# Performance work log

Hardware: AMD Instinct MI355X
Metric: run time of the kernel (lower is better)

## Reference

```python
import jax, jax.numpy as jnp
import numpy as np

N_NODES = 50000
N_EDGES = 800000
ALPHA = 0.2  # LeakyReLU negative slope


def setup_inputs() -> dict:
    key = jax.random.key(0)
    ks = jax.random.split(key, 12)
    F_IN, H, D, NOUT = 256, 8, 64, 64

    def xavier(k, shape):
        fan_in, fan_out = shape[-2], shape[-1]
        limit = np.sqrt(6.0 / (fan_in + fan_out)).astype(np.float32)
        return jax.random.uniform(k, shape, jnp.float32, -limit, limit)

    x = jax.random.normal(ks[0], (N_NODES, F_IN), jnp.float32)
    edge_src = jnp.sort(jax.random.randint(ks[1], (N_EDGES,), 0, N_NODES, jnp.int32))
    edge_dst = jax.random.randint(ks[2], (N_EDGES,), 0, N_NODES, jnp.int32)
    return {
        'x': x,
        'edge_src': edge_src,
        'edge_dst': edge_dst,
        'W1': xavier(ks[3], (H, F_IN, D)),
        'a_src1': xavier(ks[4], (H, D, 1))[..., 0],
        'a_dst1': xavier(ks[5], (H, D, 1))[..., 0],
        'W2': xavier(ks[6], (H, H * D, D)),
        'a_src2': xavier(ks[7], (H, D, 1))[..., 0],
        'a_dst2': xavier(ks[8], (H, D, 1))[..., 0],
        'lin_W': xavier(ks[9], (H * D, NOUT)),
        'lin_b': jnp.zeros((NOUT,), jnp.float32),
    }


def _gat_layer(x, W, a_s, a_d, src, dst, n_nodes):
    # W: [H, F, D]; x: [N, F]
    Wh = jnp.einsum('nf,hfd->nhd', x, W)                  # [N, H, D]
    f1 = jnp.einsum('nhd,hd->nh', Wh, a_s)                # score from row node
    f2 = jnp.einsum('nhd,hd->nh', Wh, a_d)                # score from col node
    e = f1[src] + f2[dst]                                 # [E, H]
    e = jnp.where(e > 0, e, ALPHA * e)                    # LeakyReLU
    # sparse softmax over neighbors of each row (dim=1 in torch.sparse.softmax)
    m = jax.ops.segment_max(e, src, num_segments=n_nodes)
    m = jnp.where(jnp.isfinite(m), m, 0.0)                # guard empty segments
    p = jnp.exp(e - m[src])
    s = jax.ops.segment_sum(p, src, num_segments=n_nodes)
    att = p / jnp.maximum(s[src], 1e-16)                  # [E, H]
    # spmm: per-head to cap the [E, D] message buffer
    H = W.shape[0]
    outs = []
    for h in range(H):
        msg = att[:, h:h + 1] * Wh[dst, h, :]             # [E, D]
        outs.append(jax.ops.segment_sum(msg, src, num_segments=n_nodes))
    hp = jnp.stack(outs, axis=1)                          # [N, H, D]
    hp = jax.nn.elu(hp)
    return hp.reshape(n_nodes, -1)                        # concat heads -> [N, H*D]


def reference(x, edge_src, edge_dst, W1, a_src1, a_dst1, W2, a_src2, a_dst2, lin_W, lin_b):
    n = x.shape[0]
    h = _gat_layer(x, W1, a_src1, a_dst1, edge_src, edge_dst, n)
    h = _gat_layer(h, W2, a_src2, a_dst2, edge_src, edge_dst, n)
    return h @ lin_W + lin_b                              # [N, nout]
```

## Files before the change

### kernel.cpp

```cpp
#include <hip/hip_runtime.h>
#include <hip/hip_bf16.h>
#include <math.h>

#define ALPHA 0.2f
#define N_NODES 50000
#define N_EDGES 800000
#define HEADS 8
#define DH 64
#define HD 512
#define DCAP 128

typedef __attribute__((ext_vector_type(8))) short short8v;
typedef __attribute__((ext_vector_type(4))) float float4v;

__device__ __forceinline__ unsigned short f2bf(float f) {
    unsigned int u = __float_as_uint(f);
    unsigned int r = (u + 0x7fffu + ((u >> 16) & 1u)) >> 16;
    return (unsigned short)r;
}
__device__ __forceinline__ float bf2f(unsigned short h) {
    return __uint_as_float(((unsigned int)h) << 16);
}

__device__ __forceinline__ void gl_lds16(const unsigned short* g, unsigned short* l) {
    __builtin_amdgcn_global_load_lds(
        (const __attribute__((address_space(1))) unsigned int*)(g),
        (__attribute__((address_space(3))) unsigned int*)(l),
        16, 0, 0);
}

__global__ void build_rowptr(const int* __restrict__ src, int E, int n_nodes,
                             int* __restrict__ row_ptr) {
    int n = blockIdx.x * blockDim.x + threadIdx.x;
    if (n > n_nodes) return;
    int lo = 0, hi = E;
    while (lo < hi) {
        int mid = (lo + hi) >> 1;
        if (src[mid] < n) lo = mid + 1; else hi = mid;
    }
    row_ptr[n] = lo;
}

__global__ __launch_bounds__(256) void cast_bf16(
    const float* __restrict__ in, unsigned short* __restrict__ out, int total8) {
    int i = blockIdx.x * 256 + threadIdx.x;
    if (i >= total8) return;
    const float4* p = reinterpret_cast<const float4*>(in + (size_t)i * 8);
    float4 v0 = p[0], v1 = p[1];
    float vv[8] = {v0.x, v0.y, v0.z, v0.w, v1.x, v1.y, v1.z, v1.w};
    short8v o;
    #pragma unroll
    for (int q = 0; q < 8; ++q) o[q] = (short)f2bf(vv[q]);
    *reinterpret_cast<short8v*>(out + (size_t)i * 8) = o;
}

__global__ void transpose_w_bf(const float* __restrict__ in,
                               unsigned short* __restrict__ outB,
                               int F, int total) {
    int idx = blockIdx.x * 256 + threadIdx.x;
    if (idx >= total) return;
    int d = idx & 63;
    int f = (idx >> 6) % F;
    int h = idx / (F << 6);
    outB[(size_t)((h << 6) + d) * F + f] = f2bf(in[idx]);
}

__global__ __launch_bounds__(256) void gemm_bf16(
    const unsigned short* __restrict__ A,
    const unsigned short* __restrict__ B,
    const float* __restrict__ bias,
    float* __restrict__ C, unsigned short* __restrict__ Cbf,
    int M, int K, int N)
{
    __shared__ unsigned short As[128][64];
    __shared__ unsigned short Bs[128][64];

    const int tid = threadIdx.x;
    const int bm = blockIdx.x * 128;
    const int bn = blockIdx.y * 128;
    const int wid = tid >> 6;
    const int lane = tid & 63;

    const int wr = (wid >> 1) * 64;
    const int wc = (wid & 1) * 64;
    const int fr = lane & 15;
    const int fks = (lane >> 4) * 8;

    const int a_r = lane >> 3;
    const int a_c = 8 * ((lane & 7) ^ a_r);

    float4v acc[4][4];
    #pragma unroll
    for (int m = 0; m < 4; ++m)
        #pragma unroll
        for (int n = 0; n < 4; ++n)
            acc[m][n] = (float4v){0.f, 0.f, 0.f, 0.f};

    for (int k0 = 0; k0 < K; k0 += 64) {
        #pragma unroll
        for (int i = 0; i < 4; ++i) {
            int g = wid * 4 + i;
            int row = bm + g * 8 + a_r; if (row >= M) row = M - 1;
            gl_lds16(&A[(size_t)row * K + k0 + a_c], &As[g * 8][0]);
        }
        #pragma unroll
        for (int i = 0; i < 4; ++i) {
            int g = wid * 4 + i;
            int row = bn + g * 8 + a_r; if (row >= N) row = N - 1;
            gl_lds16(&B[(size_t)row * K + k0 + a_c], &Bs[g * 8][0]);
        }
        __syncthreads();

        #pragma unroll
        for (int ks = 0; ks < 2; ++ks) {
            const int fko = ks * 32 + fks;
            short8v aF[4], bF[4];
            #pragma unroll
            for (int m = 0; m < 4; ++m) {
                int rr = wr + m * 16 + fr;
                aF[m] = *reinterpret_cast<const short8v*>(&As[rr][fko ^ ((rr & 7) * 8)]);
            }
            #pragma unroll
            for (int n = 0; n < 4; ++n) {
                int cc = wc + n * 16 + fr;
                bF[n] = *reinterpret_cast<const short8v*>(&Bs[cc][fko ^ ((cc & 7) * 8)]);
            }
            #pragma unroll
            for (int m = 0; m < 4; ++m)
                #pragma unroll
                for (int n = 0; n < 4; ++n)
                    acc[m][n] = __builtin_amdgcn_mfma_f32_16x16x32_bf16(aF[m], bF[n], acc[m][n], 0, 0, 0);
        }
        __syncthreads();
    }

    #pragma unroll
    for (int m = 0; m < 4; ++m) {
        int row0 = bm + wr + m * 16 + (lane >> 4) * 4;
        #pragma unroll
        for (int n = 0; n < 4; ++n) {
            int col = bn + wc + n * 16 + fr;
            if (col >= N) continue;
            float b = bias ? bias[col] : 0.f;
            #pragma unroll
            for (int r = 0; r < 4; ++r) {
                int row = row0 + r;
                if (row < M) {
                    if (Cbf) Cbf[(size_t)row * N + col] = f2bf(acc[m][n][r]);
                    else     C[(size_t)row * N + col] = acc[m][n][r] + b;
                }
            }
        }
    }
}

__global__ __launch_bounds__(256) void node_scores_wave(
    const unsigned short* __restrict__ Wh, const float* __restrict__ a_s,
    const float* __restrict__ a_d, float* __restrict__ f1,
    float* __restrict__ f2, int n_nodes)
{
    const int wv = threadIdx.x >> 6;
    const int lane = threadIdx.x & 63;
    const int n = blockIdx.x * 4 + wv;
    if (n >= n_nodes) return;

    const int hl = lane >> 3;
    const int dg = (lane & 7) * 8;

    uint4 u = *reinterpret_cast<const uint4*>(&Wh[(size_t)n * HD + hl * DH + dg]);
    float4 s0 = *reinterpret_cast<const float4*>(&a_s[hl * DH + dg]);
    float4 s1 = *reinterpret_cast<const float4*>(&a_s[hl * DH + dg + 4]);
    float4 d0 = *reinterpret_cast<const float4*>(&a_d[hl * DH + dg]);
    float4 d1 = *reinterpret_cast<const float4*>(&a_d[hl * DH + dg + 4]);

    unsigned int uu[4] = {u.x, u.y, u.z, u.w};
    float w[8];
    #pragma unroll
    for (int q = 0; q < 4; ++q) {
        w[2 * q]     = __uint_as_float(uu[q] << 16);
        w[2 * q + 1] = __uint_as_float(uu[q] & 0xffff0000u);
    }
    float sv[8] = {s0.x, s0.y, s0.z, s0.w, s1.x, s1.y, s1.z, s1.w};
    float dv[8] = {d0.x, d0.y, d0.z, d0.w, d1.x, d1.y, d1.z, d1.w};

    float v1 = 0.f, v2 = 0.f;
    #pragma unroll
    for (int q = 0; q < 8; ++q) {
        v1 += w[q] * sv[q];
        v2 += w[q] * dv[q];
    }
    #pragma unroll
    for (int m = 1; m <= 4; m <<= 1) {
        v1 += __shfl_xor(v1, m);
        v2 += __shfl_xor(v2, m);
    }
    if ((lane & 7) == 0) {
        f1[(size_t)n * HEADS + hl] = v1;
        f2[(size_t)n * HEADS + hl] = v2;
    }
}

__global__ __launch_bounds__(256) void gat_node_wave(
    const unsigned short* __restrict__ Wh, const float* __restrict__ f1,
    const float* __restrict__ f2, const int* __restrict__ row_ptr,
    const int* __restrict__ dst, unsigned short* __restrict__ out, int n_nodes)
{
    __shared__ float s_p[4][DCAP][HEADS];
    __shared__ int   s_dst[4][DCAP];

    const int wv = threadIdx.x >> 6;
    const int lane = threadIdx.x & 63;
    const int n = blockIdx.x * 4 + wv;
    if (n >= n_nodes) return;

    const int lo = row_ptr[n], hi = row_ptr[n + 1];
    const int deg = hi - lo;

    const int h  = lane & 7;
    const int j8 = lane >> 3;
    const int hl = lane >> 3;
    const int dg = (lane & 7) * 8;
    const size_t base = (size_t)hl * DH + dg;

    const float f1h = f1[(size_t)n * HEADS + h];

    float m = -INFINITY;
    for (int b0 = 0; b0 < deg; b0 += 8) {
        int j = b0 + j8;
        float e = -INFINITY;
        if (j < deg) {
            int dn = dst[lo + j];
            e = f1h + f2[(size_t)dn * HEADS + h];
            e = e > 0.f ? e : ALPHA * e;
        }
        m = fmaxf(m, e);
    }
    #pragma unroll
    for (int mk = 8; mk <= 32; mk <<= 1) m = fmaxf(m, __shfl_xor(m, mk));

    float ssum = 0.f;
    float acc[8] = {0.f, 0.f, 0.f, 0.f, 0.f, 0.f, 0.f, 0.f};

    for (int c0 = 0; c0 < deg; c0 += DCAP) {
        int cn = min(DCAP, deg - c0);
        for (int b0 = 0; b0 < cn; b0 += 8) {
            int j = b0 + j8;
            float p = 0.f;
            if (j < cn) {
                int dn = dst[lo + c0 + j];
                float e = f1h + f2[(size_t)dn * HEADS + h];
                e = e > 0.f ? e : ALPHA * e;
                p = __expf(e - m);
                s_p[wv][j][h] = p;
                if (h == 0) s_dst[wv][j] = dn;
            }
            ssum += p;
        }
        asm volatile("s_waitcnt lgkmcnt(0)" ::: "memory");

        int j = 0;
        for (; j + 4 <= cn; j += 4) {
            int dn0 = s_dst[wv][j + 0];
            int dn1 = s_dst[wv][j + 1];
            int dn2 = s_dst[wv][j + 2];
            int dn3 = s_dst[wv][j + 3];
            float p0 = s_p[wv][j + 0][hl];
            float p1 = s_p[wv][j + 1][hl];
            float p2 = s_p[wv][j + 2][hl];
            float p3 = s_p[wv][j + 3][hl];
            uint4 u0 = *reinterpret_cast<const uint4*>(&Wh[(size_t)dn0 * HD + base]);
            uint4 u1 = *reinterpret_cast<const uint4*>(&Wh[(size_t)dn1 * HD + base]);
            uint4 u2 = *reinterpret_cast<const uint4*>(&Wh[(size_t)dn2 * HD + base]);
            uint4 u3 = *reinterpret_cast<const uint4*>(&Wh[(size_t)dn3 * HD + base]);
            unsigned int w0[4] = {u0.x, u0.y, u0.z, u0.w};
            unsigned int w1[4] = {u1.x, u1.y, u1.z, u1.w};
            unsigned int w2[4] = {u2.x, u2.y, u2.z, u2.w};
            unsigned int w3[4] = {u3.x, u3.y, u3.z, u3.w};
            #pragma unroll
            for (int q = 0; q < 4; ++q) {
                acc[2 * q]     += p0 * __uint_as_float(w0[q] << 16);
                acc[2 * q + 1] += p0 * __uint_as_float(w0[q] & 0xffff0000u);
                acc[2 * q]     += p1 * __uint_as_float(w1[q] << 16);
                acc[2 * q + 1] += p1 * __uint_as_float(w1[q] & 0xffff0000u);
                acc[2 * q]     += p2 * __uint_as_float(w2[q] << 16);
                acc[2 * q + 1] += p2 * __uint_as_float(w2[q] & 0xffff0000u);
                acc[2 * q]     += p3 * __uint_as_float(w3[q] << 16);
                acc[2 * q + 1] += p3 * __uint_as_float(w3[q] & 0xffff0000u);
            }
        }
        for (; j < cn; ++j) {
            int dn = s_dst[wv][j];
            float p = s_p[wv][j][hl];
            uint4 u = *reinterpret_cast<const uint4*>(&Wh[(size_t)dn * HD + base]);
            unsigned int uu[4] = {u.x, u.y, u.z, u.w};
            #pragma unroll
            for (int q = 0; q < 4; ++q) {
                acc[2 * q]     += p * __uint_as_float(uu[q] << 16);
                acc[2 * q + 1] += p * __uint_as_float(uu[q] & 0xffff0000u);
            }
        }
        asm volatile("s_waitcnt lgkmcnt(0)" ::: "memory");
    }

    #pragma unroll
    for (int mk = 8; mk <= 32; mk <<= 1) ssum += __shfl_xor(ssum, mk);
    float inv = 1.f / fmaxf(ssum, 1e-16f);
    float invg = __shfl(inv, hl);

    short8v o8;
    #pragma unroll
    for (int q = 0; q < 8; ++q) {
        float v = acc[q] * invg;
        v = v > 0.f ? v : expm1f(v);
        o8[q] = (short)f2bf(v);
    }
    *reinterpret_cast<short8v*>(&out[(size_t)n * HD + hl * DH + dg]) = o8;
}

extern "C" void kernel_launch(void* const* d_in, const int* in_sizes, int n_in,
                              void* d_out, int out_size, void* d_ws, size_t ws_size,
                              hipStream_t stream) {
    const float* x      = (const float*)d_in[0];
    const int*   e_src  = (const int*)d_in[1];
    const int*   e_dst  = (const int*)d_in[2];
    const float* W1     = (const float*)d_in[3];
    const float* a_src1 = (const float*)d_in[4];
    const float* a_dst1 = (const float*)d_in[5];
    const float* W2     = (const float*)d_in[6];
    const float* a_src2 = (const float*)d_in[7];
    const float* a_dst2 = (const float*)d_in[8];
    const float* lin_W  = (const float*)d_in[9];
    const float* lin_b  = (const float*)d_in[10];
    float* outp = (float*)d_out;

    const size_t NHD = (size_t)N_NODES * HD;
    unsigned short* WhBf = (unsigned short*)d_ws;
    unsigned short* hBf  = WhBf + NHD;
    unsigned short* xBf  = hBf + NHD;
    float* f1    = (float*)(xBf + (size_t)N_NODES * 256);
    float* f2    = f1 + (size_t)N_NODES * HEADS;
    int* rowptr  = (int*)(f2 + (size_t)N_NODES * HEADS);
    unsigned short* BtW1  = (unsigned short*)(rowptr + N_NODES + 64);
    unsigned short* BtW2  = BtW1 + (size_t)HD * 256;
    unsigned short* BtLin = BtW2 + (size_t)HD * HD;

    build_rowptr<<<(N_NODES + 256) / 256, 256, 0, stream>>>(e_src, N_EDGES, N_NODES, rowptr);
    cast_bf16<<<(N_NODES * 256 / 8 + 255) / 256, 256, 0, stream>>>(x, xBf, N_NODES * 256 / 8);
    transpose_w_bf<<<(HEADS * 256 * DH + 255) / 256, 256, 0, stream>>>(W1, BtW1, 256, HEADS * 256 * DH);
    transpose_w_bf<<<(HEADS * HD * DH + 255) / 256, 256, 0, stream>>>(W2, BtW2, HD, HEADS * HD * DH);
    transpose_w_bf<<<(HD * 64 + 255) / 256, 256, 0, stream>>>(lin_W, BtLin, HD, HD * 64);

    const int nwb = (N_NODES + 3) / 4;
    dim3 g1((N_NODES + 127) / 128, HD / 128);

    gemm_bf16<<<g1, 256, 0, stream>>>(xBf, BtW1, nullptr, nullptr, WhBf, N_NODES, 256, HD);
    node_scores_wave<<<nwb, 256, 0, stream>>>(WhBf, a_src1, a_dst1, f1, f2, N_NODES);
    gat_node_wave<<<nwb, 256, 0, stream>>>(WhBf, f1, f2, rowptr, e_dst, hBf, N_NODES);

    gemm_bf16<<<g1, 256, 0, stream>>>(hBf, BtW2, nullptr, nullptr, WhBf, N_NODES, HD, HD);
    node_scores_wave<<<nwb, 256, 0, stream>>>(WhBf, a_src2, a_dst2, f1, f2, N_NODES);
    gat_node_wave<<<nwb, 256, 0, stream>>>(WhBf, f1, f2, rowptr, e_dst, hBf, N_NODES);

    dim3 g3((N_NODES + 127) / 128, 1);
    gemm_bf16<<<g3, 256, 0, stream>>>(hBf, BtLin, lin_b, outp, nullptr, N_NODES, HD, 64);
}
```

Before: 443.0 us.

## Fuse attention score computation into GEMM epilogue and widen GEMM tile

Removes the separate node_scores_wave kernel. The per-head source and destination attention scores are now computed directly from the fp32 MFMA accumulators in the GEMM epilogue, using a 16-lane shuffle reduction, so the bf16 Wh matrix no longer has to be re-read from memory twice per layer. The GEMM moves to a 128x256 tile with 512 threads so each wave owns exactly one head's 64 columns. The trade-off is that the final N=64 linear GEMM runs with most waves doing redundant work on clamped rows, and the larger block may reduce occupancy.

```diff
diff --git a/kernel.cpp b/kernel.cpp
--- a/kernel.cpp
+++ b/kernel.cpp
@@ -65,24 +65,26 @@
     outB[(size_t)((h << 6) + d) * F + f] = f2bf(in[idx]);
 }
 
-__global__ __launch_bounds__(256) void gemm_bf16(
+__global__ __launch_bounds__(512) void gemm_bf16_fused(
     const unsigned short* __restrict__ A,
     const unsigned short* __restrict__ B,
     const float* __restrict__ bias,
     float* __restrict__ C, unsigned short* __restrict__ Cbf,
+    const float* __restrict__ a_s, const float* __restrict__ a_d,
+    float* __restrict__ f1out, float* __restrict__ f2out,
     int M, int K, int N)
 {
     __shared__ unsigned short As[128][64];
-    __shared__ unsigned short Bs[128][64];
+    __shared__ unsigned short Bs[256][64];
 
     const int tid = threadIdx.x;
     const int bm = blockIdx.x * 128;
-    const int bn = blockIdx.y * 128;
+    const int bn = blockIdx.y * 256;
     const int wid = tid >> 6;
     const int lane = tid & 63;
 
-    const int wr = (wid >> 1) * 64;
-    const int wc = (wid & 1) * 64;
+    const int wr = (wid >> 2) * 64;
+    const int wc = (wid & 3) * 64;
     const int fr = lane & 15;
     const int fks = (lane >> 4) * 8;
 
@@ -98,8 +100,8 @@
 
     for (int k0 = 0; k0 < K; k0 += 64) {
         #pragma unroll
-        for (int i = 0; i < 4; ++i) {
-            int g = wid * 4 + i;
+        for (int i = 0; i < 2; ++i) {
+            int g = wid * 2 + i;
             int row = bm + g * 8 + a_r; if (row >= M) row = M - 1;
             gl_lds16(&A[(size_t)row * K + k0 + a_c], &As[g * 8][0]);
         }
@@ -132,6 +134,38 @@
                     acc[m][n] = __builtin_amdgcn_mfma_f32_16x16x32_bf16(aF[m], bF[n], acc[m][n], 0, 0, 0);
         }
         __syncthreads();
+    }
+
+    if (f1out) {
+        const int head = (bn + wc) >> 6;
+        float asv[4], adv[4];
+        #pragma unroll
+        for (int n = 0; n < 4; ++n) {
+            asv[n] = a_s[bn + wc + n * 16 + fr];
+            adv[n] = a_d[bn + wc + n * 16 + fr];
+        }
+        #pragma unroll
+        for (int m = 0; m < 4; ++m) {
+            #pragma unroll
+            for (int r = 0; r < 4; ++r) {
+                float ps = 0.f, pd = 0.f;
+                #pragma unroll
+                for (int n = 0; n < 4; ++n) {
+                    ps += acc[m][n][r] * asv[n];
+                    pd += acc[m][n][r] * adv[n];
+                }
+                #pragma unroll
+                for (int mk = 1; mk <= 8; mk <<= 1) {
+                    ps += __shfl_xor(ps, mk);
+                    pd += __shfl_xor(pd, mk);
+                }
+                int row = bm + wr + m * 16 + (lane >> 4) * 4 + r;
+                if (fr == 0 && row < M) {
+                    f1out[(size_t)row * HEADS + head] = ps;
+                    f2out[(size_t)row * HEADS + head] = pd;
+                }
+            }
+        }
     }
 
     #pragma unroll
@@ -151,52 +185,6 @@
                 }
             }
         }
-    }
-}
-
-__global__ __launch_bounds__(256) void node_scores_wave(
-    const unsigned short* __restrict__ Wh, const float* __restrict__ a_s,
-    const float* __restrict__ a_d, float* __restrict__ f1,
-    float* __restrict__ f2, int n_nodes)
-{
-    const int wv = threadIdx.x >> 6;
-    const int lane = threadIdx.x & 63;
-    const int n = blockIdx.x * 4 + wv;
-    if (n >= n_nodes) return;
-
-    const int hl = lane >> 3;
-    const int dg = (lane & 7) * 8;
-
-    uint4 u = *reinterpret_cast<const uint4*>(&Wh[(size_t)n * HD + hl * DH + dg]);
-    float4 s0 = *reinterpret_cast<const float4*>(&a_s[hl * DH + dg]);
-    float4 s1 = *reinterpret_cast<const float4*>(&a_s[hl * DH + dg + 4]);
-    float4 d0 = *reinterpret_cast<const float4*>(&a_d[hl * DH + dg]);
-    float4 d1 = *reinterpret_cast<const float4*>(&a_d[hl * DH + dg + 4]);
-
-    unsigned int uu[4] = {u.x, u.y, u.z, u.w};
-    float w[8];
-    #pragma unroll
-    for (int q = 0; q < 4; ++q) {
-        w[2 * q]     = __uint_as_float(uu[q] << 16);
-        w[2 * q + 1] = __uint_as_float(uu[q] & 0xffff0000u);
-    }
-    float sv[8] = {s0.x, s0.y, s0.z, s0.w, s1.x, s1.y, s1.z, s1.w};
-    float dv[8] = {d0.x, d0.y, d0.z, d0.w, d1.x, d1.y, d1.z, d1.w};
-
-    float v1 = 0.f, v2 = 0.f;
-    #pragma unroll
-    for (int q = 0; q < 8; ++q) {
-        v1 += w[q] * sv[q];
-        v2 += w[q] * dv[q];
-    }
-    #pragma unroll
-    for (int m = 1; m <= 4; m <<= 1) {
-        v1 += __shfl_xor(v1, m);
-        v2 += __shfl_xor(v2, m);
-    }
-    if ((lane & 7) == 0) {
-        f1[(size_t)n * HEADS + hl] = v1;
-        f2[(size_t)n * HEADS + hl] = v2;
     }
 }
 
@@ -351,16 +339,17 @@
     transpose_w_bf<<<(HD * 64 + 255) / 256, 256, 0, stream>>>(lin_W, BtLin, HD, HD * 64);
 
     const int nwb = (N_NODES + 3) / 4;
-    dim3 g1((N_NODES + 127) / 128, HD / 128);
-
-    gemm_bf16<<<g1, 256, 0, stream>>>(xBf, BtW1, nullptr, nullptr, WhBf, N_NODES, 256, HD);
-    node_scores_wave<<<nwb, 256, 0, stream>>>(WhBf, a_src1, a_dst1, f1, f2, N_NODES);
+    dim3 g1((N_NODES + 127) / 128, HD / 256);
+
+    gemm_bf16_fused<<<g1, 512, 0, stream>>>(xBf, BtW1, nullptr, nullptr, WhBf,
+                                            a_src1, a_dst1, f1, f2, N_NODES, 256, HD);
     gat_node_wave<<<nwb, 256, 0, stream>>>(WhBf, f1, f2, rowptr, e_dst, hBf, N_NODES);
 
-    gemm_bf16<<<g1, 256, 0, stream>>>(hBf, BtW2, nullptr, nullptr, WhBf, N_NODES, HD, HD);
-    node_scores_wave<<<nwb, 256, 0, stream>>>(WhBf, a_src2, a_dst2, f1, f2, N_NODES);
+    gemm_bf16_fused<<<g1, 512, 0, stream>>>(hBf, BtW2, nullptr, nullptr, WhBf,
+                                            a_src2, a_dst2, f1, f2, N_NODES, HD, HD);
     gat_node_wave<<<nwb, 256, 0, stream>>>(WhBf, f1, f2, rowptr, e_dst, hBf, N_NODES);
 
     dim3 g3((N_NODES + 127) / 128, 1);
-    gemm_bf16<<<g3, 256, 0, stream>>>(hBf, BtLin, lin_b, outp, nullptr, N_NODES, HD, 64);
-}
+    gemm_bf16_fused<<<g3, 512, 0, stream>>>(hBf, BtLin, lin_b, outp, nullptr,
+                                            nullptr, nullptr, nullptr, nullptr, N_NODES, HD, 64);
+}
```

Result: faster. 397.8 us (-10.2%).
